# Performance work log

Hardware: AMD Instinct MI355X
Metric: run time of the kernel (lower is better)

The kernel has to match this reference:

```python
import jax, jax.numpy as jnp
import numpy as np

DIM = 2048
N_HEADS = 32
N_KV_HEADS = 8
HEAD_DIM = 64
N_REP = N_HEADS // N_KV_HEADS
SEQ = 2048
BATCH = 1


def _llama3_scaled_rope(head_dim, end, base=10000.0, scale_factor=8):
    # matches executorch precompute_freqs_cis with use_scaled=True
    freqs = 1.0 / (base ** (np.arange(0, head_dim, 2)[: head_dim // 2] / head_dim))
    low_freq_factor, high_freq_factor, old_ctx = 1.0, 4.0, 8192.0
    low_wl = old_ctx / low_freq_factor
    high_wl = old_ctx / high_freq_factor
    wavelen = 2.0 * np.pi / freqs
    smooth = (old_ctx / wavelen - low_freq_factor) / (high_freq_factor - low_freq_factor)
    scaled = np.where(
        wavelen < high_wl,
        freqs,
        np.where(wavelen > low_wl, freqs / scale_factor,
                 (1.0 - smooth) * freqs / scale_factor + smooth * freqs),
    )
    t = np.arange(end, dtype=np.float64)
    ang = np.outer(t, scaled)
    return np.cos(ang).astype(np.float32), np.sin(ang).astype(np.float32)


def setup_inputs() -> dict:
    key = jax.random.key(0)
    kx, kq, kk, kv, ko = jax.random.split(key, 5)
    x = jax.random.normal(kx, (BATCH, SEQ, DIM), dtype=jnp.float32)
    sc = 0.02
    wq = jax.random.normal(kq, (N_HEADS * HEAD_DIM, DIM), dtype=jnp.float32) * sc
    wk = jax.random.normal(kk, (N_KV_HEADS * HEAD_DIM, DIM), dtype=jnp.float32) * sc
    wv = jax.random.normal(kv, (N_KV_HEADS * HEAD_DIM, DIM), dtype=jnp.float32) * sc
    wo = jax.random.normal(ko, (N_HEADS * HEAD_DIM, DIM), dtype=jnp.float32).T * sc
    cos, sin = _llama3_scaled_rope(HEAD_DIM, SEQ)
    return {"x": x, "freqs_cos": jnp.asarray(cos), "freqs_sin": jnp.asarray(sin),
            "wq": wq, "wk": wk, "wv": wv, "wo": wo}


def _apply_rotary(x, cos, sin):
    # x: [b, s, h, hd]; cos/sin: [s, hd//2]; interleaved-pair RoPE
    xr = x[..., 0::2]
    xi = x[..., 1::2]
    c = cos[None, :, None, :]
    s = sin[None, :, None, :]
    out_r = xr * c - xi * s
    out_i = xr * s + xi * c
    return jnp.stack([out_r, out_i], axis=-1).reshape(x.shape)


def reference(x, freqs_cos, freqs_sin, wq, wk, wv, wo):
    b, s, _ = x.shape
    q = (x @ wq.T).reshape(b, s, N_HEADS, HEAD_DIM)
    k = (x @ wk.T).reshape(b, s, N_KV_HEADS, HEAD_DIM)
    v = (x @ wv.T).reshape(b, s, N_KV_HEADS, HEAD_DIM)
    q = _apply_rotary(q, freqs_cos, freqs_sin)
    k = _apply_rotary(k, freqs_cos, freqs_sin)
    # [b, h, s, hd]
    q = q.transpose(0, 2, 1, 3)
    k = k.transpose(0, 2, 1, 3)
    v = v.transpose(0, 2, 1, 3)
    # GQA: repeat_interleave over head dim
    k = jnp.repeat(k, N_REP, axis=1)
    v = jnp.repeat(v, N_REP, axis=1)
    scale = 1.0 / jnp.sqrt(jnp.asarray(HEAD_DIM, dtype=x.dtype))
    scores = jnp.einsum("bhqd,bhkd->bhqk", q, k) * scale
    causal = jnp.tril(jnp.ones((s, s), dtype=bool))
    scores = jnp.where(causal[None, None], scores, jnp.finfo(scores.dtype).min)
    attn = jax.nn.softmax(scores, axis=-1)
    y = jnp.einsum("bhqk,bhkd->bhqd", attn, v)
    y = y.transpose(0, 2, 1, 3).reshape(b, s, N_HEADS * HEAD_DIM)
    return y @ wo.T
```

## Files before the change

kernel.cpp:

```cpp
#include <hip/hip_runtime.h>
#include <hip/hip_bf16.h>

typedef __attribute__((ext_vector_type(8))) __bf16 bf16x8;
typedef __attribute__((ext_vector_type(4))) __bf16 bf16x4;
typedef __attribute__((ext_vector_type(4))) float f32x4;

#define DIM 2048
#define SEQ 2048
#define NH 32
#define NKV 8
#define HD 64
#define QKVD 3072
#define KOFF 2048
#define VOFF 2560
#define KVDIM 512

__device__ __forceinline__ void gld16(const __bf16* g, __bf16* l) {
    __builtin_amdgcn_global_load_lds(
        (const __attribute__((address_space(1))) void*)g,
        (__attribute__((address_space(3))) void*)l, 16, 0, 0);
}

__global__ __launch_bounds__(256) void cvt_all(const float* __restrict__ x,
                                               const float* __restrict__ wq,
                                               const float* __restrict__ wk,
                                               const float* __restrict__ wv,
                                               const float* __restrict__ wo,
                                               __bf16* __restrict__ xb,
                                               __bf16* __restrict__ wqkvb,
                                               __bf16* __restrict__ wob) {
    const int i = blockIdx.x * blockDim.x + threadIdx.x;
    const int NX = SEQ * DIM / 4;
    const int NW = DIM * DIM / 4;
    const int NKV4 = KVDIM * DIM / 4;
    const float* src; __bf16* dst; int off;
    if (i < NX)                        { src = x;  dst = xb;    off = i; }
    else if (i < NX + NW)              { src = wq; dst = wqkvb; off = i - NX; }
    else if (i < NX + NW + NKV4)       { src = wk; dst = wqkvb + (size_t)KOFF * DIM; off = i - NX - NW; }
    else if (i < NX + NW + 2 * NKV4)   { src = wv; dst = wqkvb + (size_t)VOFF * DIM; off = i - NX - NW - NKV4; }
    else                               { src = wo; dst = wob;   off = i - NX - NW - 2 * NKV4; }
    float4 v = reinterpret_cast<const float4*>(src)[off];
    bf16x4 o;
    o[0] = (__bf16)v.x; o[1] = (__bf16)v.y; o[2] = (__bf16)v.z; o[3] = (__bf16)v.w;
    reinterpret_cast<bf16x4*>(dst)[off] = o;
}

template <typename OutT, bool ROPE>
__global__ __launch_bounds__(512, 6) void gemm_tn(const __bf16* __restrict__ A,
                                                  const __bf16* __restrict__ B,
                                                  OutT* __restrict__ C,
                                                  int M, int N, int K,
                                                  float scale, int scaleNlim,
                                                  const float* __restrict__ fc,
                                                  const float* __restrict__ fs,
                                                  __bf16* __restrict__ VTout) {
    __shared__ __align__(16) __bf16 As[2][128 * 64];
    __shared__ __align__(16) __bf16 Bs[2][64 * 64];
    const int tid = threadIdx.x;
    const int lane = tid & 63;
    const int w = tid >> 6;
    const int l15 = lane & 15, lhi = lane >> 4;
    const int mb = blockIdx.y * 128;
    const int nb = blockIdx.x * 64;
    const int wm = (w >> 1) * 32, wn = (w & 1) * 32;

    const int sr8 = lane >> 3;
    const int sc8 = ((lane & 7) ^ sr8) * 8;
    const int arow0 = w * 16;
    const int brow0 = w * 8;
    const __bf16* gA0 = A + (size_t)(mb + arow0 + sr8) * K + sc8;
    const __bf16* gA1 = A + (size_t)(mb + arow0 + 8 + sr8) * K + sc8;
    const __bf16* gB  = B + (size_t)(nb + brow0 + sr8) * K + sc8;

    auto stage = [&](int kk, int buf) {
        gld16(gA0 + kk, As[buf] + arow0 * 64);
        gld16(gA1 + kk, As[buf] + (arow0 + 8) * 64);
        gld16(gB + kk, Bs[buf] + brow0 * 64);
    };

    stage(0, 0);
    __syncthreads();

    f32x4 acc[2][2] = {};
    int cur = 0;
    for (int kk = 0; kk < K; kk += 64, cur ^= 1) {
        if (kk + 64 < K) stage(kk + 64, cur ^ 1);
#pragma unroll
        for (int s = 0; s < 2; ++s) {
            bf16x8 a[2], b[2];
#pragma unroll
            for (int i = 0; i < 2; ++i) {
                const int row = wm + i * 16 + l15;
                const int slot = (s * 4 + lhi) ^ (row & 7);
                a[i] = *reinterpret_cast<const bf16x8*>(&As[cur][row * 64 + slot * 8]);
            }
#pragma unroll
            for (int j = 0; j < 2; ++j) {
                const int row = wn + j * 16 + l15;
                const int slot = (s * 4 + lhi) ^ (row & 7);
                b[j] = *reinterpret_cast<const bf16x8*>(&Bs[cur][row * 64 + slot * 8]);
            }
#pragma unroll
            for (int i = 0; i < 2; ++i)
#pragma unroll
                for (int j = 0; j < 2; ++j)
                    acc[i][j] = __builtin_amdgcn_mfma_f32_16x16x32_bf16(a[i], b[j], acc[i][j], 0, 0, 0);
        }
        __syncthreads();
    }

    const bool toVT = ROPE && (VTout != nullptr) && (nb >= VOFF);
    if (toVT) {
#pragma unroll
        for (int i = 0; i < 2; ++i)
#pragma unroll
            for (int j = 0; j < 2; ++j) {
                bf16x4 pv;
#pragma unroll
                for (int r = 0; r < 4; ++r) pv[r] = (__bf16)acc[i][j][r];
                const int colv = nb - VOFF + wn + j * 16 + l15;
                const int row0 = mb + wm + i * 16 + lhi * 4;
                *reinterpret_cast<bf16x4*>(VTout + (size_t)colv * M + row0) = pv;
            }
    } else {
        const float sc = (nb < scaleNlim) ? scale : 1.0f;
        const bool doRope = ROPE && (nb < VOFF);
#pragma unroll
        for (int i = 0; i < 2; ++i)
#pragma unroll
            for (int j = 0; j < 2; ++j)
#pragma unroll
                for (int r = 0; r < 4; ++r) {
                    float v = acc[i][j][r] * sc;
                    if (doRope) {
                        const int col = nb + wn + j * 16 + l15;
                        const int row = mb + wm + i * 16 + lhi * 4 + r;
                        const float vp = __shfl_xor(v, 1);
                        const int fi = (col & 63) >> 1;
                        const float cc = fc[row * 32 + fi];
                        const float ss = fs[row * 32 + fi];
                        v = (col & 1) ? (vp * ss + v * cc) : (v * cc - vp * ss);
                    }
                    C[(size_t)(mb + wm + i * 16 + lhi * 4 + r) * N + nb + wn + j * 16 + l15] = (OutT)v;
                }
    }
}

__global__ __launch_bounds__(256, 4) void attn_kernel(const __bf16* __restrict__ QKV,
                                                      const __bf16* __restrict__ VT,
                                                      __bf16* __restrict__ Nlo,
                                                      __bf16* __restrict__ Nhi,
                                                      float* __restrict__ Llo,
                                                      float* __restrict__ Lhi) {
    const int bx = blockIdx.x;
    const int qt = 31 - (bx >> 6);
    const int h = (bx >> 1) & 31;
    const int half = bx & 1;
    const int kvh = h >> 2;
    const int tid = threadIdx.x;
    const int lane = tid & 63;
    const int w = tid >> 6;
    const int l15 = lane & 15, lhi = lane >> 4;

    __shared__ __align__(16) __bf16 Kl[2][64 * 64];
    __shared__ __align__(16) __bf16 Vl[2][64 * 64];
    __shared__ __align__(16) __bf16 Pl[4][16 * 64];

    const __bf16* Qp = QKV + h * HD;
    const __bf16* Kp = QKV + KOFF + kvh * HD;
    const __bf16* Vth = VT + (size_t)(kvh * HD) * SEQ;

    const int sr = lane >> 3;
    const int ksc = ((lane & 7) ^ sr) * 8;
    const int rswz = (l15 & 7);

    auto stage = [&](int jt, int buf) {
        const int kvb = jt * 64;
#pragma unroll
        for (int c = 0; c < 2; ++c) {
            const int row = w * 16 + c * 8;
            gld16(Kp + (size_t)(kvb + row + sr) * QKVD + ksc, &Kl[buf][row * 64]);
            gld16(Vth + (size_t)(row + sr) * SEQ + kvb + ksc, &Vl[buf][row * 64]);
        }
    };

    const int qb = qt * 64;
    const int qrow = qb + w * 16 + l15;

    const int nlo = (qt + 2) >> 1;
    const int j0 = half ? nlo : 0;
    const int j1 = half ? (qt + 1) : nlo;

    const __bf16* qptr = Qp + (size_t)qrow * QKVD;
    bf16x8 qf0 = *reinterpret_cast<const bf16x8*>(qptr + lhi * 8);
    bf16x8 qf1 = *reinterpret_cast<const bf16x8*>(qptr + 32 + lhi * 8);

    bf16x8 ones1;
#pragma unroll
    for (int i = 0; i < 8; ++i) ones1[i] = (__bf16)1.0f;

    f32x4 o[4] = {};
    f32x4 oS = {};

    const int pkey = (l15 & 7) << 1;

    stage(j0, 0);
    __syncthreads();

    int cur = 0;
    for (int j = j0; j < j1; ++j, cur ^= 1) {
        const bool pre = (j + 1 < j1);
        if (pre) stage(j + 1, cur ^ 1);

        f32x4 sacc[4];
        __builtin_amdgcn_s_setprio(1);
#pragma unroll
        for (int t = 0; t < 4; ++t) {
            const int rb = (t * 16 + l15) * 64;
            bf16x8 kf0 = *reinterpret_cast<const bf16x8*>(
                &Kl[cur][rb + ((lhi ^ rswz) * 8)]);
            bf16x8 kf1 = *reinterpret_cast<const bf16x8*>(
                &Kl[cur][rb + (((4 + lhi) ^ rswz) * 8)]);
            f32x4 z = {0.f, 0.f, 0.f, 0.f};
            z = __builtin_amdgcn_mfma_f32_16x16x32_bf16(kf0, qf0, z, 0, 0, 0);
            z = __builtin_amdgcn_mfma_f32_16x16x32_bf16(kf1, qf1, z, 0, 0, 0);
            sacc[t] = z;
        }
        __builtin_amdgcn_s_setprio(0);

        if (j == qt) {
#pragma unroll
            for (int t = 0; t < 4; ++t)
#pragma unroll
                for (int r = 0; r < 4; ++r) {
                    const int kv = j * 64 + t * 16 + lhi * 4 + r;
                    if (kv > qrow) sacc[t][r] = -1e30f;
                }
        }

#pragma unroll
        for (int t = 0; t < 4; ++t) {
            bf16x4 pk;
#pragma unroll
            for (int r = 0; r < 4; ++r)
                pk[r] = (__bf16)exp2f(sacc[t][r]);
            const int sw = (t * 4 + lhi) ^ pkey;
            *reinterpret_cast<bf16x4*>(&Pl[w][l15 * 64 + sw * 4]) = pk;
        }

        bf16x8 pf0 = *reinterpret_cast<const bf16x8*>(
            &Pl[w][l15 * 64 + (((lhi * 2) ^ pkey) * 4)]);
        bf16x8 pf1 = *reinterpret_cast<const bf16x8*>(
            &Pl[w][l15 * 64 + (((8 + lhi * 2) ^ pkey) * 4)]);
        __builtin_amdgcn_s_setprio(1);
#pragma unroll
        for (int t = 0; t < 4; ++t) {
            const int rb = (t * 16 + l15) * 64;
            bf16x8 vf0 = *reinterpret_cast<const bf16x8*>(
                &Vl[cur][rb + ((lhi ^ rswz) * 8)]);
            bf16x8 vf1 = *reinterpret_cast<const bf16x8*>(
                &Vl[cur][rb + (((4 + lhi) ^ rswz) * 8)]);
            o[t] = __builtin_amdgcn_mfma_f32_16x16x32_bf16(pf0, vf0, o[t], 0, 0, 0);
            o[t] = __builtin_amdgcn_mfma_f32_16x16x32_bf16(pf1, vf1, o[t], 0, 0, 0);
        }
        oS = __builtin_amdgcn_mfma_f32_16x16x32_bf16(pf0, ones1, oS, 0, 0, 0);
        oS = __builtin_amdgcn_mfma_f32_16x16x32_bf16(pf1, ones1, oS, 0, 0, 0);
        __builtin_amdgcn_s_setprio(0);

        __syncthreads();
    }

    __bf16* N = half ? Nhi : Nlo;
    float* L = half ? Lhi : Llo;
#pragma unroll
    for (int t = 0; t < 4; ++t)
#pragma unroll
        for (int r = 0; r < 4; ++r)
            N[(size_t)(qb + w * 16 + lhi * 4 + r) * DIM + h * HD + t * 16 + l15] =
                (__bf16)o[t][r];
    if (l15 == 0) {
#pragma unroll
        for (int r = 0; r < 4; ++r)
            L[(size_t)(qb + w * 16 + lhi * 4 + r) * NH + h] = oS[r];
    }
}

__global__ __launch_bounds__(256) void merge_attn(const __bf16* __restrict__ Nhi,
                                                  const float* __restrict__ Llo,
                                                  const float* __restrict__ Lhi,
                                                  __bf16* __restrict__ Y) {
    const int i = blockIdx.x * 256 + threadIdx.x;
    const int s = i >> 8;
    const int c8 = (i & 255) * 8;
    const int h = c8 >> 6;
    const float rl = 1.0f / (Llo[(size_t)s * NH + h] + Lhi[(size_t)s * NH + h]);
    bf16x8 a = *reinterpret_cast<const bf16x8*>(Y + (size_t)s * DIM + c8);
    bf16x8 b = *reinterpret_cast<const bf16x8*>(Nhi + (size_t)s * DIM + c8);
    bf16x8 y;
#pragma unroll
    for (int e = 0; e < 8; ++e)
        y[e] = (__bf16)(((float)a[e] + (float)b[e]) * rl);
    *reinterpret_cast<bf16x8*>(Y + (size_t)s * DIM + c8) = y;
}

extern "C" void kernel_launch(void* const* d_in, const int* in_sizes, int n_in,
                              void* d_out, int out_size, void* d_ws, size_t ws_size,
                              hipStream_t stream) {
    const float* x    = (const float*)d_in[0];
    const float* fcos = (const float*)d_in[1];
    const float* fsin = (const float*)d_in[2];
    const float* wq   = (const float*)d_in[3];
    const float* wk   = (const float*)d_in[4];
    const float* wv   = (const float*)d_in[5];
    const float* wo   = (const float*)d_in[6];
    float* out = (float*)d_out;

    __bf16* xb    = (__bf16*)d_ws;
    __bf16* wqkvb = xb + (size_t)SEQ * DIM;
    __bf16* wob   = wqkvb + (size_t)QKVD * DIM;
    __bf16* QKVb  = wob + (size_t)DIM * DIM;
    __bf16* Yb    = QKVb + (size_t)SEQ * QKVD;
    __bf16* VTb   = Yb + (size_t)SEQ * DIM;
    __bf16* Nhi   = VTb + (size_t)KVDIM * SEQ;
    float*  Llo   = (float*)(Nhi + (size_t)SEQ * DIM);
    float*  Lhi   = Llo + (size_t)SEQ * NH;

    const int ncvt = (SEQ * DIM / 4) + 2 * (DIM * DIM / 4) + 2 * (KVDIM * DIM / 4);
    cvt_all<<<ncvt / 256, 256, 0, stream>>>(x, wq, wk, wv, wo, xb, wqkvb, wob);

    gemm_tn<__bf16, true><<<dim3(QKVD / 64, SEQ / 128), 512, 0, stream>>>(
        xb, wqkvb, QKVb, SEQ, QKVD, DIM, 0.125f * 1.4426950408889634f, KOFF,
        fcos, fsin, VTb);

    attn_kernel<<<dim3(2048), 256, 0, stream>>>(QKVb, VTb, Yb, Nhi, Llo, Lhi);

    merge_attn<<<dim3(SEQ * DIM / 8 / 256), 256, 0, stream>>>(Nhi, Llo, Lhi, Yb);

    gemm_tn<float, false><<<dim3(DIM / 64, SEQ / 128), 512, 0, stream>>>(
        Yb, wob, out, SEQ, DIM, DIM, 1.0f, 0, nullptr, nullptr, nullptr);
}
```

Baseline: 125.6 us.

## Triple-buffer K and stagger K/V prefetch with explicit vmcnt waits in attention

The attention loop now stages K two tiles ahead in a three-slot buffer and V one tile ahead, replacing the single __syncthreads with fine-grained s_waitcnt vmcnt waits and raw barriers. QK^T can start as soon as K lands, and the V wait is deferred until just before the PV MFMAs, hiding more global load latency. The extra LDS for the third K buffer comes with lowering the launch-bounds occupancy hint from 4 to 3 blocks per CU. The hand-counted vmcnt values and clamped redundant loads at the tail risk subtle races if the counts are wrong.

Result: slower. 130.0 us (+3.5%).

```diff
diff --git a/kernel.cpp b/kernel.cpp
--- a/kernel.cpp
+++ b/kernel.cpp
@@ -146,7 +146,7 @@
     }
 }
 
-__global__ __launch_bounds__(256, 4) void attn_kernel(const __bf16* __restrict__ QKV,
+__global__ __launch_bounds__(256, 3) void attn_kernel(const __bf16* __restrict__ QKV,
                                                       const __bf16* __restrict__ VT,
                                                       __bf16* __restrict__ Nlo,
                                                       __bf16* __restrict__ Nhi,
@@ -162,7 +162,7 @@
     const int w = tid >> 6;
     const int l15 = lane & 15, lhi = lane >> 4;
 
-    __shared__ __align__(16) __bf16 Kl[2][64 * 64];
+    __shared__ __align__(16) __bf16 Kl[3][64 * 64];
     __shared__ __align__(16) __bf16 Vl[2][64 * 64];
     __shared__ __align__(16) __bf16 Pl[4][16 * 64];
 
@@ -174,12 +174,19 @@
     const int ksc = ((lane & 7) ^ sr) * 8;
     const int rswz = (l15 & 7);
 
-    auto stage = [&](int jt, int buf) {
+    auto stageK = [&](int jt, int buf) {
         const int kvb = jt * 64;
 #pragma unroll
         for (int c = 0; c < 2; ++c) {
             const int row = w * 16 + c * 8;
             gld16(Kp + (size_t)(kvb + row + sr) * QKVD + ksc, &Kl[buf][row * 64]);
+        }
+    };
+    auto stageV = [&](int jt, int buf) {
+        const int kvb = jt * 64;
+#pragma unroll
+        for (int c = 0; c < 2; ++c) {
+            const int row = w * 16 + c * 8;
             gld16(Vth + (size_t)(row + sr) * SEQ + kvb + ksc, &Vl[buf][row * 64]);
         }
     };
@@ -204,23 +211,31 @@
 
     const int pkey = (l15 & 7) << 1;
 
-    stage(j0, 0);
-    __syncthreads();
-
-    int cur = 0;
-    for (int j = j0; j < j1; ++j, cur ^= 1) {
-        const bool pre = (j + 1 < j1);
-        if (pre) stage(j + 1, cur ^ 1);
-
+    stageK(j0, j0 % 3);
+    stageV(j0, j0 & 1);
+    {
+        const int jk1 = (j0 + 1 < j1) ? j0 + 1 : j1 - 1;
+        stageK(jk1, (j0 + 1) % 3);
+    }
+    asm volatile("s_waitcnt vmcnt(2)" ::: "memory");
+    __builtin_amdgcn_sched_barrier(0);
+    __builtin_amdgcn_s_barrier();
+    __builtin_amdgcn_sched_barrier(0);
+
+    for (int j = j0; j < j1; ++j) {
+        const int jv = (j + 1 < j1) ? j + 1 : j1 - 1;
+        const int jk = (j + 2 < j1) ? j + 2 : j1 - 1;
+        stageV(jv, (j + 1) & 1);
+        stageK(jk, (j + 2) % 3);
+
+        const __bf16* Kb = Kl[j % 3];
         f32x4 sacc[4];
         __builtin_amdgcn_s_setprio(1);
 #pragma unroll
         for (int t = 0; t < 4; ++t) {
             const int rb = (t * 16 + l15) * 64;
-            bf16x8 kf0 = *reinterpret_cast<const bf16x8*>(
-                &Kl[cur][rb + ((lhi ^ rswz) * 8)]);
-            bf16x8 kf1 = *reinterpret_cast<const bf16x8*>(
-                &Kl[cur][rb + (((4 + lhi) ^ rswz) * 8)]);
+            bf16x8 kf0 = *reinterpret_cast<const bf16x8*>(&Kb[rb + ((lhi ^ rswz) * 8)]);
+            bf16x8 kf1 = *reinterpret_cast<const bf16x8*>(&Kb[rb + (((4 + lhi) ^ rswz) * 8)]);
             f32x4 z = {0.f, 0.f, 0.f, 0.f};
             z = __builtin_amdgcn_mfma_f32_16x16x32_bf16(kf0, qf0, z, 0, 0, 0);
             z = __builtin_amdgcn_mfma_f32_16x16x32_bf16(kf1, qf1, z, 0, 0, 0);
@@ -248,6 +263,10 @@
             *reinterpret_cast<bf16x4*>(&Pl[w][l15 * 64 + sw * 4]) = pk;
         }
 
+        asm volatile("s_waitcnt vmcnt(6)" ::: "memory");
+        __builtin_amdgcn_sched_barrier(0);
+
+        const __bf16* Vb = Vl[j & 1];
         bf16x8 pf0 = *reinterpret_cast<const bf16x8*>(
             &Pl[w][l15 * 64 + (((lhi * 2) ^ pkey) * 4)]);
         bf16x8 pf1 = *reinterpret_cast<const bf16x8*>(
@@ -256,10 +275,8 @@
 #pragma unroll
         for (int t = 0; t < 4; ++t) {
             const int rb = (t * 16 + l15) * 64;
-            bf16x8 vf0 = *reinterpret_cast<const bf16x8*>(
-                &Vl[cur][rb + ((lhi ^ rswz) * 8)]);
-            bf16x8 vf1 = *reinterpret_cast<const bf16x8*>(
-                &Vl[cur][rb + (((4 + lhi) ^ rswz) * 8)]);
+            bf16x8 vf0 = *reinterpret_cast<const bf16x8*>(&Vb[rb + ((lhi ^ rswz) * 8)]);
+            bf16x8 vf1 = *reinterpret_cast<const bf16x8*>(&Vb[rb + (((4 + lhi) ^ rswz) * 8)]);
             o[t] = __builtin_amdgcn_mfma_f32_16x16x32_bf16(pf0, vf0, o[t], 0, 0, 0);
             o[t] = __builtin_amdgcn_mfma_f32_16x16x32_bf16(pf1, vf1, o[t], 0, 0, 0);
         }
@@ -267,7 +284,10 @@
         oS = __builtin_amdgcn_mfma_f32_16x16x32_bf16(pf1, ones1, oS, 0, 0, 0);
         __builtin_amdgcn_s_setprio(0);
 
-        __syncthreads();
+        asm volatile("s_waitcnt vmcnt(4)" ::: "memory");
+        __builtin_amdgcn_sched_barrier(0);
+        __builtin_amdgcn_s_barrier();
+        __builtin_amdgcn_sched_barrier(0);
     }
 
     __bf16* N = half ? Nhi : Nlo;
```
